# Performance work log

Hardware: AMD Instinct MI355X
Metric: run time of the kernel (lower is better)

The kernel has to match this reference:

```python
import jax, jax.numpy as jnp
import numpy as np

SCALE = 10.0
DIM = 512
DIM_HEAD = 64
HEADS = DIM // DIM_HEAD
LN_EPS = 1e-05
L2_EPS = 1e-12


def l2norm(t, axis=1):
    # Faithful to source: default axis=1 (token axis for [b, n, h, d] tensors)
    denom = jnp.clip(jnp.linalg.norm(t, ord=2, axis=axis, keepdims=True), L2_EPS)
    return t / denom


def setup_inputs() -> dict:
    key = jax.random.key(0)
    k1, k2, k3 = jax.random.split(key, 3)
    B, H, W, C = 8, 32, 32, 512
    x = jax.random.normal(k1, (B, H, W, C), dtype=jnp.float32)
    ln_scale = jnp.ones((C,), dtype=jnp.float32)
    # 1x1 convs == channel matmuls; fan-in scaled init
    w_qkv = jax.random.normal(k2, (C, 3 * DIM), dtype=jnp.float32) / np.sqrt(C)
    w_out = jax.random.normal(k3, (DIM, C), dtype=jnp.float32) / np.sqrt(DIM)
    b_out = jnp.zeros((C,), dtype=jnp.float32)
    return {"x": x, "ln_scale": ln_scale, "w_qkv": w_qkv, "w_out": w_out, "b_out": b_out}


def reference(x, ln_scale, w_qkv, w_out, b_out):
    B, H, W, C = x.shape
    N = H * W
    # LayerNorm over channels (use_bias=False, use_scale=True)
    mean = jnp.mean(x, axis=-1, keepdims=True)
    var = jnp.mean(jnp.square(x - mean), axis=-1, keepdims=True)
    y = (x - mean) * jax.lax.rsqrt(var + LN_EPS) * ln_scale
    # 1x1 conv QKV projection (no bias)
    qkv = jnp.einsum('bhwc,cf->bhwf', y, w_qkv)  # [B,H,W,3*DIM]
    q, k, v = jnp.split(qkv, 3, axis=-1)
    # b x y (h d) -> b (x y) h d
    def to_tokens(t):
        return t.reshape(B, N, HEADS, DIM_HEAD)
    q, k, v = map(to_tokens, (q, k, v))
    # l2norm over axis=1 (token axis), faithful to source default
    q = l2norm(q)
    k = l2norm(k)
    sim = jnp.einsum('bihd,bjhd->bhij', q, k) * SCALE  # [B,heads,N,N]
    attn = jax.nn.softmax(sim, axis=-1)
    out = jnp.einsum('bhij,bjhd->bhid', attn, v)  # [B,heads,N,d]
    # b h (x y) d -> b x y (h d)
    out = out.transpose(0, 2, 1, 3).reshape(B, H, W, HEADS * DIM_HEAD)
    # 1x1 output conv (with bias)
    out = jnp.einsum('bhwf,fc->bhwc', out, w_out) + b_out
    return out
```

## Files before the change

kernel.cpp:

```cpp
#include <hip/hip_runtime.h>

typedef __bf16 bf16x8 __attribute__((ext_vector_type(8)));
typedef float f32x4 __attribute__((ext_vector_type(4)));
typedef float f32x16 __attribute__((ext_vector_type(16)));

#define DEV static __device__ __forceinline__

DEV unsigned short f2bf(float f) {
    union { __bf16 h; unsigned short s; } c; c.h = (__bf16)f; return c.s;
}
DEV float bf2f(unsigned short h) {
    union { unsigned u; float f; } c; c.u = ((unsigned)h) << 16; return c.f;
}
DEV unsigned packbf2(float a, float b) {
    union { __bf16 h[2]; unsigned u; } c;
    c.h[0] = (__bf16)a; c.h[1] = (__bf16)b; return c.u;
}

DEV f32x4 mfma16(bf16x8 a, bf16x8 b, f32x4 c) {
    return __builtin_amdgcn_mfma_f32_16x16x32_bf16(a, b, c, 0, 0, 0);
}
DEV f32x16 mfma32(bf16x8 a, bf16x8 b, f32x16 c) {
    return __builtin_amdgcn_mfma_f32_32x32x16_bf16(a, b, c, 0, 0, 0);
}

#define GLOAD16(gp, lp)                                                        \
    __builtin_amdgcn_global_load_lds(                                          \
        (const __attribute__((address_space(1))) unsigned int*)(gp),           \
        (__attribute__((address_space(3))) unsigned int*)(lp), 16, 0, 0)

__global__ __launch_bounds__(256) void ln_conv_kernel(const float* __restrict__ x,
                                                      const float* __restrict__ lnsc,
                                                      unsigned short* __restrict__ y,
                                                      float* __restrict__ ssq,
                                                      const float* __restrict__ wqkv,
                                                      const float* __restrict__ wout,
                                                      unsigned short* __restrict__ wqkvt,
                                                      unsigned short* __restrict__ woutt) {
    const int t = threadIdx.x;
    if (blockIdx.x >= 2048) {
        __shared__ __bf16 tile[64][65];
        const int wblk = blockIdx.x - 2048;
        const float* src;
        unsigned short* dst;
        int ldsrc, k0, f0;
        if (wblk < 192) {
            src = wqkv; dst = wqkvt; ldsrc = 1536;
            k0 = (wblk / 24) * 64; f0 = (wblk % 24) * 64;
        } else {
            int w2 = wblk - 192;
            src = wout; dst = woutt; ldsrc = 512;
            k0 = (w2 >> 3) * 64; f0 = (w2 & 7) * 64;
        }
#pragma unroll
        for (int j = 0; j < 16; j++) {
            int idx = t + j * 256;
            int a = idx >> 6, b2 = idx & 63;
            tile[b2][a] = (__bf16)src[(size_t)(k0 + a) * ldsrc + f0 + b2];
        }
        __syncthreads();
#pragma unroll
        for (int j = 0; j < 16; j++) {
            int idx = t + j * 256;
            int fb = idx >> 6, kc = idx & 63;
            union { __bf16 h; unsigned short s; } cv;
            cv.h = tile[fb][kc];
            dst[(size_t)(f0 + fb) * 512 + k0 + kc] = cv.s;
        }
        return;
    }
    if (blockIdx.x < 32) ssq[(blockIdx.x << 8) | t] = 0.0f;
    const int token = blockIdx.x * 4 + (t >> 6);
    const int lane = t & 63;
    const float4* xp = (const float4*)(x + (size_t)token * 512 + lane * 8);
    float4 v0 = xp[0], v1 = xp[1];
    float s = v0.x + v0.y + v0.z + v0.w + v1.x + v1.y + v1.z + v1.w;
    float s2 = v0.x * v0.x + v0.y * v0.y + v0.z * v0.z + v0.w * v0.w +
               v1.x * v1.x + v1.y * v1.y + v1.z * v1.z + v1.w * v1.w;
#pragma unroll
    for (int off = 1; off < 64; off <<= 1) {
        s += __shfl_xor(s, off);
        s2 += __shfl_xor(s2, off);
    }
    const float mean = s * (1.0f / 512.0f);
    const float var = s2 * (1.0f / 512.0f) - mean * mean;
    const float rstd = rsqrtf(var + 1e-5f);
    const float4* sp = (const float4*)(lnsc + lane * 8);
    float4 sc0 = sp[0], sc1 = sp[1];
    union { __bf16 h[8]; uint4 v; } pk;
    pk.h[0] = (__bf16)((v0.x - mean) * rstd * sc0.x);
    pk.h[1] = (__bf16)((v0.y - mean) * rstd * sc0.y);
    pk.h[2] = (__bf16)((v0.z - mean) * rstd * sc0.z);
    pk.h[3] = (__bf16)((v0.w - mean) * rstd * sc0.w);
    pk.h[4] = (__bf16)((v1.x - mean) * rstd * sc1.x);
    pk.h[5] = (__bf16)((v1.y - mean) * rstd * sc1.y);
    pk.h[6] = (__bf16)((v1.z - mean) * rstd * sc1.z);
    pk.h[7] = (__bf16)((v1.w - mean) * rstd * sc1.w);
    *(uint4*)(y + (size_t)token * 512 + lane * 8) = pk.v;
}

template <int WM, int WN, int NCOLS, bool OUT_BF16, bool BIAS, bool SSQ, bool VT,
          bool DB>
__global__ __launch_bounds__(256) void gemm_bt(const unsigned short* __restrict__ A,
                                               const unsigned short* __restrict__ Bt,
                                               void* __restrict__ Cout,
                                               const float* __restrict__ bias,
                                               float* __restrict__ ssq,
                                               unsigned short* __restrict__ vt,
                                               int M, int K) {
    constexpr int BM = 2 * WM, BN = 2 * WN;
    constexpr int ASZ = BM * 64 * 2, BSZ = BN * 64 * 2;
    constexpr int NLA = WM / 16, NLB = WN / 16;
    constexpr int NBUF = DB ? 2 : 1;
    constexpr int STG = NBUF * (ASZ + BSZ);
    constexpr int TTB = VT ? 128 * 136 * 2 : 0;
    constexpr int LDSB = STG > TTB ? STG : TTB;
    __shared__ __align__(16) char smem[LDSB];
    const int t = threadIdx.x;
    const int w = t >> 6, lane = t & 63;
    const int g = lane >> 4, l15 = lane & 15;
    const int wr = w >> 1, wc = w & 1;
    const int bR = blockIdx.x, bC = blockIdx.y;
    f32x4 acc[NLA][NLB] = {};
    const size_t ldb = (size_t)K * 2;
    const char* Ag = (const char*)A + (size_t)bR * BM * ldb;
    const char* Bg = (const char*)Bt + (size_t)bC * BN * ldb;

#define GSTAGE(buf, kt_)                                                            \
    {                                                                               \
        char* Ad = smem + (buf) * (ASZ + BSZ);                                      \
        char* Bd = Ad + ASZ;                                                        \
        _Pragma("unroll") for (int i = 0; i < NLA; i++) {                           \
            int o = i * 4096 + t * 16;                                              \
            int row = o >> 7, kb = (o & 127) ^ ((row & 7) << 4);                    \
            GLOAD16(Ag + (size_t)row * ldb + (size_t)(kt_) * 2 + kb, Ad + o);       \
        }                                                                           \
        _Pragma("unroll") for (int i = 0; i < NLB; i++) {                           \
            int o = i * 4096 + t * 16;                                              \
            int row = o >> 7, kb = (o & 127) ^ ((row & 7) << 4);                    \
            GLOAD16(Bg + (size_t)row * ldb + (size_t)(kt_) * 2 + kb, Bd + o);       \
        }                                                                           \
    }

#define GCOMPUTE(buf)                                                               \
    {                                                                               \
        const char* Ab = smem + (buf) * (ASZ + BSZ);                                \
        const char* Bb = Ab + ASZ;                                                  \
        _Pragma("unroll") for (int kk = 0; kk < 64; kk += 32) {                     \
            bf16x8 a[NLA], bb[NLB];                                                 \
            _Pragma("unroll") for (int m = 0; m < NLA; m++) {                       \
                int row = wr * WM + m * 16 + l15;                                   \
                int kb = ((kk + g * 8) * 2) ^ ((row & 7) << 4);                     \
                a[m] = *(const bf16x8*)(Ab + row * 128 + kb);                       \
            }                                                                       \
            _Pragma("unroll") for (int n = 0; n < NLB; n++) {                       \
                int row = wc * WN + n * 16 + l15;                                   \
                int kb = ((kk + g * 8) * 2) ^ ((row & 7) << 4);                     \
                bb[n] = *(const bf16x8*)(Bb + row * 128 + kb);                      \
            }                                                                       \
            _Pragma("unroll") for (int m = 0; m < NLA; m++)                         \
                _Pragma("unroll") for (int n = 0; n < NLB; n++)                     \
                    acc[m][n] = mfma16(a[m], bb[n], acc[m][n]);                     \
        }                                                                           \
    }

    const int NT = K >> 6;
    if constexpr (DB) {
        GSTAGE(0, 0)
        for (int tt = 0; tt < NT; ++tt) {
            const int cur = tt & 1;
            if (tt + 1 < NT) {
                GSTAGE(cur ^ 1, (tt + 1) * 64)
                asm volatile("s_waitcnt vmcnt(%0)" ::"n"(NLA + NLB) : "memory");
            } else {
                asm volatile("s_waitcnt vmcnt(0)" ::: "memory");
            }
            __builtin_amdgcn_s_barrier();
            GCOMPUTE(cur)
            __builtin_amdgcn_s_barrier();
        }
    } else {
        for (int tt = 0; tt < NT; ++tt) {
            __syncthreads();
            GSTAGE(0, tt * 64)
            asm volatile("s_waitcnt vmcnt(0)" ::: "memory");
            __syncthreads();
            GCOMPUTE(0)
        }
    }
#undef GSTAGE
#undef GCOMPUTE

    const int rbase = bR * BM + wr * WM;
    const int cbase = bC * BN + wc * WN;
    if (!VT || bC < 8) {
#pragma unroll
        for (int m = 0; m < NLA; m++)
#pragma unroll
            for (int n = 0; n < NLB; n++)
#pragma unroll
                for (int r = 0; r < 4; r++) {
                    int row = rbase + m * 16 + g * 4 + r;
                    int col = cbase + n * 16 + l15;
                    float v = acc[m][n][r];
                    if constexpr (OUT_BF16)
                        ((unsigned short*)Cout)[(size_t)row * NCOLS + col] = f2bf(v);
                    else
                        ((float*)Cout)[(size_t)row * NCOLS + col] =
                            v + (BIAS ? bias[col] : 0.f);
                }
    }
    if constexpr (SSQ) {
        if (bC < 8) {
            const int bb2 = bR >> 3;
#pragma unroll
            for (int n = 0; n < NLB; n++) {
                float ps = 0.f;
#pragma unroll
                for (int m = 0; m < NLA; m++)
#pragma unroll
                    for (int r = 0; r < 4; r++) ps += acc[m][n][r] * acc[m][n][r];
                ps += __shfl_xor(ps, 16);
                ps += __shfl_xor(ps, 32);
                if (g == 0)
                    atomicAdd(&ssq[bb2 * 1024 + cbase + n * 16 + l15], ps);
            }
        }
    }
    if constexpr (VT) {
        if (bC >= 8) {
            unsigned short* TT = (unsigned short*)smem;
            __syncthreads();
#pragma unroll
            for (int m = 0; m < NLA; m++)
#pragma unroll
                for (int n = 0; n < NLB; n++)
#pragma unroll
                    for (int r = 0; r < 4; r++) {
                        int row = wr * WM + m * 16 + g * 4 + r;
                        int col = wc * WN + n * 16 + l15;
                        TT[col * 136 + row] = f2bf(acc[m][n][r]);
                    }
            __syncthreads();
            const int f = t >> 1, th = t & 1;
            const int fh = (bC - 8) * 128 + f;
            const int hh = fh >> 6, dd = fh & 63;
            const int bb3 = bR >> 3, nb = (bR & 7) * 128;
            unsigned short* dst =
                vt + (((size_t)bb3 * 8 + hh) * 64 + dd) * 1024 + nb + th * 64;
            const unsigned short* srcp = TT + f * 136 + th * 64;
#pragma unroll
            for (int j = 0; j < 8; j++)
                *(uint4*)(dst + j * 8) = *(const uint4*)(srcp + j * 8);
        }
    }
}

__global__ __launch_bounds__(256) void attn_kernel(const unsigned short* __restrict__ qkv,
                                                   const unsigned short* __restrict__ vt,
                                                   unsigned short* __restrict__ attnout,
                                                   const float* __restrict__ ssq) {
    __shared__ unsigned short Ks[2][4096];
    __shared__ unsigned short Vs[2][4096];
    __shared__ float smq[64];
    const int t = threadIdx.x, w = t >> 6, lane = t & 63;
    const int hi = lane >> 5, q31 = lane & 31;
    const int qt = blockIdx.y, bh = blockIdx.x;
    const int b = bh >> 3, h = bh & 7;
    const size_t qrow0 = (size_t)b * 1024 + qt * 128;
    const char* qg = (const char*)qkv;
    const char* vg = (const char*)vt;

    if (t < 64) {
        float nq = fmaxf(sqrtf(ssq[b * 1024 + h * 64 + t]), 1e-12f);
        float nk = fmaxf(sqrtf(ssq[b * 1024 + 512 + h * 64 + t]), 1e-12f);
        smq[t] = 14.42695040888963f / (nq * nk);
    }
    __syncthreads();

    bf16x8 qf[4];
#pragma unroll
    for (int ds = 0; ds < 4; ds++) {
        union { bf16x8 v; unsigned short u[8]; } in, ov;
        in.v = *(const bf16x8*)(qkv + (qrow0 + w * 32 + q31) * 1536 + h * 64 +
                                ds * 16 + hi * 8);
#pragma unroll
        for (int j = 0; j < 8; j++)
            ov.u[j] = f2bf(bf2f(in.u[j]) * smq[ds * 16 + hi * 8 + j]);
        qf[ds] = ov.v;
    }

    f32x16 accO[2] = {};
    float prs = 0.f;

#define ASTAGE(buf, tt_)                                                              \
    {                                                                                 \
        const int kt_ = (tt_) * 64;                                                   \
        _Pragma("unroll") for (int i = 0; i < 2; i++) {                               \
            int o = i * 4096 + t * 16;                                                \
            int row = o >> 7, kb = (o & 127) ^ ((row & 7) << 4);                      \
            GLOAD16(qg + ((size_t)b * 1024 + kt_ + row) * 3072 + 1024 + h * 128 + kb, \
                    (char*)Ks[buf] + o);                                              \
            GLOAD16(vg + ((size_t)bh * 64 + row) * 2048 + (size_t)kt_ * 2 + kb,       \
                    (char*)Vs[buf] + o);                                              \
        }                                                                             \
    }

    ASTAGE(0, 0)
    for (int tt = 0; tt < 16; ++tt) {
        const int cur = tt & 1;
        if (tt < 15) {
            ASTAGE(cur ^ 1, tt + 1)
            asm volatile("s_waitcnt vmcnt(4)" ::: "memory");
        } else {
            asm volatile("s_waitcnt vmcnt(0)" ::: "memory");
        }
        __builtin_amdgcn_s_barrier();

#pragma unroll
        for (int kvb = 0; kvb < 2; kvb++) {
            f32x16 sa = {};
            __builtin_amdgcn_s_setprio(1);
#pragma unroll
            for (int ds = 0; ds < 4; ds++) {
                const int krow = kvb * 32 + q31;
                const int kb = ((ds * 16 + hi * 8) * 2) ^ ((krow & 7) << 4);
                bf16x8 kf = *(const bf16x8*)((const char*)Ks[cur] + krow * 128 + kb);
                sa = mfma32(kf, qf[ds], sa);
            }
            __builtin_amdgcn_s_setprio(0);
            float p[16];
#pragma unroll
            for (int r = 0; r < 16; r++) {
                p[r] = __builtin_amdgcn_exp2f(sa[r]);
                prs += p[r];
            }
            bf16x8 pf[2];
#pragma unroll
            for (int s2 = 0; s2 < 2; s2++) {
                unsigned a0 = packbf2(p[s2 * 8 + 0], p[s2 * 8 + 1]);
                unsigned a1 = packbf2(p[s2 * 8 + 2], p[s2 * 8 + 3]);
                unsigned b0 = packbf2(p[s2 * 8 + 4], p[s2 * 8 + 5]);
                unsigned b1 = packbf2(p[s2 * 8 + 6], p[s2 * 8 + 7]);
                asm volatile("v_permlane32_swap_b32 %0, %1" : "+v"(a0), "+v"(b0));
                asm volatile("v_permlane32_swap_b32 %0, %1" : "+v"(a1), "+v"(b1));
                union { unsigned u[4]; bf16x8 v; } fr;
                fr.u[0] = a0; fr.u[1] = a1; fr.u[2] = b0; fr.u[3] = b1;
                pf[s2] = fr.v;
            }
            __builtin_amdgcn_s_setprio(1);
#pragma unroll
            for (int s2 = 0; s2 < 2; s2++)
#pragma unroll
                for (int dvb = 0; dvb < 2; dvb++) {
                    const int vrow = dvb * 32 + q31;
                    const int kb =
                        ((kvb * 32 + s2 * 16 + hi * 8) * 2) ^ ((vrow & 7) << 4);
                    bf16x8 vf = *(const bf16x8*)((const char*)Vs[cur] + vrow * 128 + kb);
                    accO[dvb] = mfma32(vf, pf[s2], accO[dvb]);
                }
            __builtin_amdgcn_s_setprio(0);
        }
        __builtin_amdgcn_s_barrier();
    }
#undef ASTAGE

    const float tot = prs + __shfl_xor(prs, 32);
    const float inv = 1.0f / tot;
    unsigned short* orow = attnout + (qrow0 + w * 32 + q31) * 512 + h * 64;
#pragma unroll
    for (int dvb = 0; dvb < 2; dvb++)
#pragma unroll
        for (int grp = 0; grp < 4; grp++) {
            float f0 = accO[dvb][grp * 4 + 0] * inv;
            float f1 = accO[dvb][grp * 4 + 1] * inv;
            float f2 = accO[dvb][grp * 4 + 2] * inv;
            float f3 = accO[dvb][grp * 4 + 3] * inv;
            uint2 pk;
            pk.x = packbf2(f0, f1);
            pk.y = packbf2(f2, f3);
            *(uint2*)(orow + dvb * 32 + grp * 8 + 4 * hi) = pk;
        }
}

extern "C" void kernel_launch(void* const* d_in, const int* in_sizes, int n_in,
                              void* d_out, int out_size, void* d_ws, size_t ws_size,
                              hipStream_t stream) {
    const float* x = (const float*)d_in[0];
    const float* ln_scale = (const float*)d_in[1];
    const float* w_qkv = (const float*)d_in[2];
    const float* w_out = (const float*)d_in[3];
    const float* b_out = (const float*)d_in[4];
    float* out = (float*)d_out;

    char* ws = (char*)d_ws;
    unsigned short* y = (unsigned short*)(ws + 0);
    unsigned short* wqkvt = (unsigned short*)(ws + 8388608);
    unsigned short* woutt = (unsigned short*)(ws + 9961472);
    unsigned short* qkv = (unsigned short*)(ws + 10485760);
    unsigned short* vt = (unsigned short*)(ws + 35651584);
    float* ssq = (float*)(ws + 44040192);
    unsigned short* attnout = (unsigned short*)(ws + 0);

    ln_conv_kernel<<<2304, 256, 0, stream>>>(x, ln_scale, y, ssq, w_qkv, w_out, wqkvt,
                                             woutt);
    gemm_bt<64, 64, 1536, true, false, true, true, false>
        <<<dim3(64, 12), 256, 0, stream>>>(y, wqkvt, qkv, nullptr, ssq, vt, 8192, 512);
    attn_kernel<<<dim3(64, 8), 256, 0, stream>>>(qkv, vt, attnout, ssq);
    gemm_bt<32, 64, 512, false, true, false, false, true>
        <<<dim3(128, 4), 256, 0, stream>>>(attnout, woutt, out, b_out, nullptr, nullptr,
                                           8192, 512);
}
```

Baseline: 71.81 us.

## Process two 32-row query blocks per wave in attention to reuse K/V fragments

Each attention block now covers 256 query rows instead of 128, with every wave handling two 32-row query sub-blocks. The K and V fragments are loaded from LDS once per kv-block and reused for both sub-blocks, which halves LDS reads and global K/V staging per query row. In exchange the grid drops from 512 to 256 blocks, which lowers occupancy and parallelism on a large GPU, and register pressure rises from the doubled accumulators and query fragments.

```diff
diff --git a/kernel.cpp b/kernel.cpp
--- a/kernel.cpp
+++ b/kernel.cpp
@@ -267,7 +267,7 @@
     const int hi = lane >> 5, q31 = lane & 31;
     const int qt = blockIdx.y, bh = blockIdx.x;
     const int b = bh >> 3, h = bh & 7;
-    const size_t qrow0 = (size_t)b * 1024 + qt * 128;
+    const size_t qrow0 = (size_t)b * 1024 + qt * 256;
     const char* qg = (const char*)qkv;
     const char* vg = (const char*)vt;
 
@@ -278,20 +278,22 @@
     }
     __syncthreads();
 
-    bf16x8 qf[4];
-#pragma unroll
-    for (int ds = 0; ds < 4; ds++) {
-        union { bf16x8 v; unsigned short u[8]; } in, ov;
-        in.v = *(const bf16x8*)(qkv + (qrow0 + w * 32 + q31) * 1536 + h * 64 +
-                                ds * 16 + hi * 8);
-#pragma unroll
-        for (int j = 0; j < 8; j++)
-            ov.u[j] = f2bf(bf2f(in.u[j]) * smq[ds * 16 + hi * 8 + j]);
-        qf[ds] = ov.v;
-    }
-
-    f32x16 accO[2] = {};
-    float prs = 0.f;
+    bf16x8 qf[2][4];
+#pragma unroll
+    for (int qb = 0; qb < 2; qb++)
+#pragma unroll
+        for (int ds = 0; ds < 4; ds++) {
+            union { bf16x8 v; unsigned short u[8]; } in, ov;
+            in.v = *(const bf16x8*)(qkv + (qrow0 + w * 64 + qb * 32 + q31) * 1536 +
+                                    h * 64 + ds * 16 + hi * 8);
+#pragma unroll
+            for (int j = 0; j < 8; j++)
+                ov.u[j] = f2bf(bf2f(in.u[j]) * smq[ds * 16 + hi * 8 + j]);
+            qf[qb][ds] = ov.v;
+        }
+
+    f32x16 accO[2][2] = {};
+    float prs[2] = {0.f, 0.f};
 
 #define ASTAGE(buf, tt_)                                                              \
     {                                                                                 \
@@ -319,36 +321,14 @@
 
 #pragma unroll
         for (int kvb = 0; kvb < 2; kvb++) {
-            f32x16 sa = {};
-            __builtin_amdgcn_s_setprio(1);
+            bf16x8 kf[4];
 #pragma unroll
             for (int ds = 0; ds < 4; ds++) {
                 const int krow = kvb * 32 + q31;
                 const int kb = ((ds * 16 + hi * 8) * 2) ^ ((krow & 7) << 4);
-                bf16x8 kf = *(const bf16x8*)((const char*)Ks[cur] + krow * 128 + kb);
-                sa = mfma32(kf, qf[ds], sa);
+                kf[ds] = *(const bf16x8*)((const char*)Ks[cur] + krow * 128 + kb);
             }
-            __builtin_amdgcn_s_setprio(0);
-            float p[16];
-#pragma unroll
-            for (int r = 0; r < 16; r++) {
-                p[r] = __builtin_amdgcn_exp2f(sa[r]);
-                prs += p[r];
-            }
-            bf16x8 pf[2];
-#pragma unroll
-            for (int s2 = 0; s2 < 2; s2++) {
-                unsigned a0 = packbf2(p[s2 * 8 + 0], p[s2 * 8 + 1]);
-                unsigned a1 = packbf2(p[s2 * 8 + 2], p[s2 * 8 + 3]);
-                unsigned b0 = packbf2(p[s2 * 8 + 4], p[s2 * 8 + 5]);
-                unsigned b1 = packbf2(p[s2 * 8 + 6], p[s2 * 8 + 7]);
-                asm volatile("v_permlane32_swap_b32 %0, %1" : "+v"(a0), "+v"(b0));
-                asm volatile("v_permlane32_swap_b32 %0, %1" : "+v"(a1), "+v"(b1));
-                union { unsigned u[4]; bf16x8 v; } fr;
-                fr.u[0] = a0; fr.u[1] = a1; fr.u[2] = b0; fr.u[3] = b1;
-                pf[s2] = fr.v;
-            }
-            __builtin_amdgcn_s_setprio(1);
+            bf16x8 vfr[2][2];
 #pragma unroll
             for (int s2 = 0; s2 < 2; s2++)
 #pragma unroll
@@ -356,31 +336,68 @@
                     const int vrow = dvb * 32 + q31;
                     const int kb =
                         ((kvb * 32 + s2 * 16 + hi * 8) * 2) ^ ((vrow & 7) << 4);
-                    bf16x8 vf = *(const bf16x8*)((const char*)Vs[cur] + vrow * 128 + kb);
-                    accO[dvb] = mfma32(vf, pf[s2], accO[dvb]);
+                    vfr[s2][dvb] =
+                        *(const bf16x8*)((const char*)Vs[cur] + vrow * 128 + kb);
                 }
-            __builtin_amdgcn_s_setprio(0);
+#pragma unroll
+            for (int qb = 0; qb < 2; qb++) {
+                f32x16 sa = {};
+                __builtin_amdgcn_s_setprio(1);
+#pragma unroll
+                for (int ds = 0; ds < 4; ds++) sa = mfma32(kf[ds], qf[qb][ds], sa);
+                __builtin_amdgcn_s_setprio(0);
+                float p[16];
+#pragma unroll
+                for (int r = 0; r < 16; r++) {
+                    p[r] = __builtin_amdgcn_exp2f(sa[r]);
+                    prs[qb] += p[r];
+                }
+                bf16x8 pf[2];
+#pragma unroll
+                for (int s2 = 0; s2 < 2; s2++) {
+                    unsigned a0 = packbf2(p[s2 * 8 + 0], p[s2 * 8 + 1]);
+                    unsigned a1 = packbf2(p[s2 * 8 + 2], p[s2 * 8 + 3]);
+                    unsigned b0 = packbf2(p[s2 * 8 + 4], p[s2 * 8 + 5]);
+                    unsigned b1 = packbf2(p[s2 * 8 + 6], p[s2 * 8 + 7]);
+                    asm volatile("v_permlane32_swap_b32 %0, %1" : "+v"(a0), "+v"(b0));
+                    asm volatile("v_permlane32_swap_b32 %0, %1" : "+v"(a1), "+v"(b1));
+                    union { unsigned u[4]; bf16x8 v; } fr;
+                    fr.u[0] = a0; fr.u[1] = a1; fr.u[2] = b0; fr.u[3] = b1;
+                    pf[s2] = fr.v;
+                }
+                __builtin_amdgcn_s_setprio(1);
+#pragma unroll
+                for (int s2 = 0; s2 < 2; s2++)
+#pragma unroll
+                    for (int dvb = 0; dvb < 2; dvb++)
+                        accO[qb][dvb] = mfma32(vfr[s2][dvb], pf[s2], accO[qb][dvb]);
+                __builtin_amdgcn_s_setprio(0);
+            }
         }
         __builtin_amdgcn_s_barrier();
     }
 #undef ASTAGE
 
-    const float tot = prs + __shfl_xor(prs, 32);
-    const float inv = 1.0f / tot;
-    unsigned short* orow = attnout + (qrow0 + w * 32 + q31) * 512 + h * 64;
-#pragma unroll
-    for (int dvb = 0; dvb < 2; dvb++)
-#pragma unroll
-        for (int grp = 0; grp < 4; grp++) {
-            float f0 = accO[dvb][grp * 4 + 0] * inv;
-            float f1 = accO[dvb][grp * 4 + 1] * inv;
-            float f2 = accO[dvb][grp * 4 + 2] * inv;
-            float f3 = accO[dvb][grp * 4 + 3] * inv;
-            uint2 pk;
-            pk.x = packbf2(f0, f1);
-            pk.y = packbf2(f2, f3);
-            *(uint2*)(orow + dvb * 32 + grp * 8 + 4 * hi) = pk;
-        }
+#pragma unroll
+    for (int qb = 0; qb < 2; qb++) {
+        const float tot = prs[qb] + __shfl_xor(prs[qb], 32);
+        const float inv = 1.0f / tot;
+        unsigned short* orow =
+            attnout + (qrow0 + w * 64 + qb * 32 + q31) * 512 + h * 64;
+#pragma unroll
+        for (int dvb = 0; dvb < 2; dvb++)
+#pragma unroll
+            for (int grp = 0; grp < 4; grp++) {
+                float f0 = accO[qb][dvb][grp * 4 + 0] * inv;
+                float f1 = accO[qb][dvb][grp * 4 + 1] * inv;
+                float f2 = accO[qb][dvb][grp * 4 + 2] * inv;
+                float f3 = accO[qb][dvb][grp * 4 + 3] * inv;
+                uint2 pk;
+                pk.x = packbf2(f0, f1);
+                pk.y = packbf2(f2, f3);
+                *(uint2*)(orow + dvb * 32 + grp * 8 + 4 * hi) = pk;
+            }
+    }
 }
 
 extern "C" void kernel_launch(void* const* d_in, const int* in_sizes, int n_in,
@@ -406,7 +423,7 @@
                                              woutt);
     gemm_bt<64, 64, 1536, true, false, true, true, false>
         <<<dim3(64, 12), 256, 0, stream>>>(y, wqkvt, qkv, nullptr, ssq, vt, 8192, 512);
-    attn_kernel<<<dim3(64, 8), 256, 0, stream>>>(qkv, vt, attnout, ssq);
+    attn_kernel<<<dim3(64, 4), 256, 0, stream>>>(qkv, vt, attnout, ssq);
     gemm_bt<32, 64, 512, false, true, false, false, true>
         <<<dim3(128, 4), 256, 0, stream>>>(attnout, woutt, out, b_out, nullptr, nullptr,
                                            8192, 512);
```

New measurement: 76.01 us. +5.8%, slower.

## Store K and V in MFMA-fragment-major layouts so attention loads are contiguous

Applied to the files above, without the earlier changes.

The QKV GEMM epilogue now writes Q to its own buffer and transposes K and V through LDS into per-head, fragment-major layouts, 16-byte chunks ordered by k-slice then token. The attention kernel can then stage K/V tiles with fully contiguous per-wave global loads and read LDS fragments without XOR swizzling. This aims to cut strided global traffic and address math in the attention loop. In exchange the GEMM epilogue does more LDS transpose work for K blocks, and the unswizzled LDS reads may hit bank conflicts.

```diff
diff --git a/kernel.cpp b/kernel.cpp
--- a/kernel.cpp
+++ b/kernel.cpp
@@ -99,21 +99,21 @@
     *(uint4*)(y + (size_t)token * 512 + lane * 8) = pk.v;
 }
 
-template <int WM, int WN, int NCOLS, bool OUT_BF16, bool BIAS, bool SSQ, bool VT,
-          bool DB>
+template <int WM, int WN, int NCOLS, bool OUT_BF16, bool BIAS, bool QKV, bool DB>
 __global__ __launch_bounds__(256) void gemm_bt(const unsigned short* __restrict__ A,
                                                const unsigned short* __restrict__ Bt,
                                                void* __restrict__ Cout,
                                                const float* __restrict__ bias,
                                                float* __restrict__ ssq,
-                                               unsigned short* __restrict__ vt,
+                                               unsigned short* __restrict__ kst,
+                                               unsigned short* __restrict__ vst,
                                                int M, int K) {
     constexpr int BM = 2 * WM, BN = 2 * WN;
     constexpr int ASZ = BM * 64 * 2, BSZ = BN * 64 * 2;
     constexpr int NLA = WM / 16, NLB = WN / 16;
     constexpr int NBUF = DB ? 2 : 1;
     constexpr int STG = NBUF * (ASZ + BSZ);
-    constexpr int TTB = VT ? 128 * 136 * 2 : 0;
+    constexpr int TTB = QKV ? 128 * 136 * 2 : 0;
     constexpr int LDSB = STG > TTB ? STG : TTB;
     __shared__ __align__(16) char smem[LDSB];
     const int t = threadIdx.x;
@@ -193,7 +193,7 @@
 
     const int rbase = bR * BM + wr * WM;
     const int cbase = bC * BN + wc * WN;
-    if (!VT || bC < 8) {
+    if (!QKV || bC < 4) {
 #pragma unroll
         for (int m = 0; m < NLA; m++)
 #pragma unroll
@@ -210,7 +210,7 @@
                             v + (BIAS ? bias[col] : 0.f);
                 }
     }
-    if constexpr (SSQ) {
+    if constexpr (QKV) {
         if (bC < 8) {
             const int bb2 = bR >> 3;
 #pragma unroll
@@ -226,10 +226,9 @@
                     atomicAdd(&ssq[bb2 * 1024 + cbase + n * 16 + l15], ps);
             }
         }
-    }
-    if constexpr (VT) {
-        if (bC >= 8) {
+        if (bC >= 4) {
             unsigned short* TT = (unsigned short*)smem;
+            const bool isK = bC < 8;
             __syncthreads();
 #pragma unroll
             for (int m = 0; m < NLA; m++)
@@ -239,25 +238,41 @@
                     for (int r = 0; r < 4; r++) {
                         int row = wr * WM + m * 16 + g * 4 + r;
                         int col = wc * WN + n * 16 + l15;
-                        TT[col * 136 + row] = f2bf(acc[m][n][r]);
+                        if (isK)
+                            TT[row * 136 + col] = f2bf(acc[m][n][r]);
+                        else
+                            TT[col * 136 + row] = f2bf(acc[m][n][r]);
                     }
             __syncthreads();
-            const int f = t >> 1, th = t & 1;
-            const int fh = (bC - 8) * 128 + f;
-            const int hh = fh >> 6, dd = fh & 63;
-            const int bb3 = bR >> 3, nb = (bR & 7) * 128;
-            unsigned short* dst =
-                vt + (((size_t)bb3 * 8 + hh) * 64 + dd) * 1024 + nb + th * 64;
-            const unsigned short* srcp = TT + f * 136 + th * 64;
-#pragma unroll
-            for (int j = 0; j < 8; j++)
-                *(uint4*)(dst + j * 8) = *(const uint4*)(srcp + j * 8);
-        }
-    }
-}
-
-__global__ __launch_bounds__(256) void attn_kernel(const unsigned short* __restrict__ qkv,
-                                                   const unsigned short* __restrict__ vt,
+            const int b2 = bR >> 3, rb = bR & 7;
+            if (isK) {
+#pragma unroll
+                for (int j = 0; j < 8; j++) {
+                    int sl = (t >> 7) + j * 2;
+                    int nl = t & 127;
+                    int hh = (bC - 4) * 2 + (sl >> 3), s = sl & 7;
+                    *(uint4*)(kst +
+                              (((size_t)(b2 * 8 + hh) * 8 + s) * 1024 + rb * 128 + nl) *
+                                  8) = *(const uint4*)(TT + nl * 136 + sl * 8);
+                }
+            } else {
+#pragma unroll
+                for (int j = 0; j < 8; j++) {
+                    int fl = t & 127;
+                    int svl = (t >> 7) + j * 2;
+                    int hh = (bC - 8) * 2 + (fl >> 6), d = fl & 63;
+                    *(uint4*)(vst +
+                              (((size_t)(b2 * 8 + hh) * 128 + rb * 16 + svl) * 64 + d) *
+                                  8) = *(const uint4*)(TT + fl * 136 + svl * 8);
+                }
+            }
+        }
+    }
+}
+
+__global__ __launch_bounds__(256) void attn_kernel(const unsigned short* __restrict__ qbuf,
+                                                   const unsigned short* __restrict__ kst,
+                                                   const unsigned short* __restrict__ vst,
                                                    unsigned short* __restrict__ attnout,
                                                    const float* __restrict__ ssq) {
     __shared__ unsigned short Ks[2][4096];
@@ -268,8 +283,8 @@
     const int qt = blockIdx.y, bh = blockIdx.x;
     const int b = bh >> 3, h = bh & 7;
     const size_t qrow0 = (size_t)b * 1024 + qt * 128;
-    const char* qg = (const char*)qkv;
-    const char* vg = (const char*)vt;
+    const char* kstb = (const char*)kst + (size_t)bh * 131072;
+    const char* vstb = (const char*)vst + (size_t)bh * 131072;
 
     if (t < 64) {
         float nq = fmaxf(sqrtf(ssq[b * 1024 + h * 64 + t]), 1e-12f);
@@ -282,7 +297,7 @@
 #pragma unroll
     for (int ds = 0; ds < 4; ds++) {
         union { bf16x8 v; unsigned short u[8]; } in, ov;
-        in.v = *(const bf16x8*)(qkv + (qrow0 + w * 32 + q31) * 1536 + h * 64 +
+        in.v = *(const bf16x8*)(qbuf + (qrow0 + w * 32 + q31) * 512 + h * 64 +
                                 ds * 16 + hi * 8);
 #pragma unroll
         for (int j = 0; j < 8; j++)
@@ -293,17 +308,16 @@
     f32x16 accO[2] = {};
     float prs = 0.f;
 
-#define ASTAGE(buf, tt_)                                                              \
-    {                                                                                 \
-        const int kt_ = (tt_) * 64;                                                   \
-        _Pragma("unroll") for (int i = 0; i < 2; i++) {                               \
-            int o = i * 4096 + t * 16;                                                \
-            int row = o >> 7, kb = (o & 127) ^ ((row & 7) << 4);                      \
-            GLOAD16(qg + ((size_t)b * 1024 + kt_ + row) * 3072 + 1024 + h * 128 + kb, \
-                    (char*)Ks[buf] + o);                                              \
-            GLOAD16(vg + ((size_t)bh * 64 + row) * 2048 + (size_t)kt_ * 2 + kb,       \
-                    (char*)Vs[buf] + o);                                              \
-        }                                                                             \
+#define ASTAGE(buf, tt_)                                                            \
+    {                                                                               \
+        _Pragma("unroll") for (int i = 0; i < 2; i++) {                             \
+            const int s = i * 4 + w;                                                \
+            const int o = i * 4096 + t * 16;                                        \
+            GLOAD16(kstb + (((size_t)s * 1024 + (tt_) * 64 + lane) << 4),           \
+                    (char*)Ks[buf] + o);                                            \
+            GLOAD16(vstb + (((size_t)(tt_) * 512 + s * 64 + lane) << 4),            \
+                    (char*)Vs[buf] + o);                                            \
+        }                                                                           \
     }
 
     ASTAGE(0, 0)
@@ -323,9 +337,9 @@
             __builtin_amdgcn_s_setprio(1);
 #pragma unroll
             for (int ds = 0; ds < 4; ds++) {
-                const int krow = kvb * 32 + q31;
-                const int kb = ((ds * 16 + hi * 8) * 2) ^ ((krow & 7) << 4);
-                bf16x8 kf = *(const bf16x8*)((const char*)Ks[cur] + krow * 128 + kb);
+                bf16x8 kf = *(const bf16x8*)((const char*)Ks[cur] +
+                                             ((ds * 2 + hi) << 10) +
+                                             ((kvb * 32 + q31) << 4));
                 sa = mfma32(kf, qf[ds], sa);
             }
             __builtin_amdgcn_s_setprio(0);
@@ -353,10 +367,9 @@
             for (int s2 = 0; s2 < 2; s2++)
 #pragma unroll
                 for (int dvb = 0; dvb < 2; dvb++) {
-                    const int vrow = dvb * 32 + q31;
-                    const int kb =
-                        ((kvb * 32 + s2 * 16 + hi * 8) * 2) ^ ((vrow & 7) << 4);
-                    bf16x8 vf = *(const bf16x8*)((const char*)Vs[cur] + vrow * 128 + kb);
+                    bf16x8 vf = *(const bf16x8*)((const char*)Vs[cur] +
+                                                 ((kvb * 4 + s2 * 2 + hi) << 10) +
+                                                 ((dvb * 32 + q31) << 4));
                     accO[dvb] = mfma32(vf, pf[s2], accO[dvb]);
                 }
             __builtin_amdgcn_s_setprio(0);
@@ -397,17 +410,19 @@
     unsigned short* y = (unsigned short*)(ws + 0);
     unsigned short* wqkvt = (unsigned short*)(ws + 8388608);
     unsigned short* woutt = (unsigned short*)(ws + 9961472);
-    unsigned short* qkv = (unsigned short*)(ws + 10485760);
-    unsigned short* vt = (unsigned short*)(ws + 35651584);
-    float* ssq = (float*)(ws + 44040192);
+    unsigned short* qbuf = (unsigned short*)(ws + 10485760);
+    unsigned short* kst = (unsigned short*)(ws + 18874368);
+    unsigned short* vst = (unsigned short*)(ws + 27262976);
+    float* ssq = (float*)(ws + 35651584);
     unsigned short* attnout = (unsigned short*)(ws + 0);
 
     ln_conv_kernel<<<2304, 256, 0, stream>>>(x, ln_scale, y, ssq, w_qkv, w_out, wqkvt,
                                              woutt);
-    gemm_bt<64, 64, 1536, true, false, true, true, false>
-        <<<dim3(64, 12), 256, 0, stream>>>(y, wqkvt, qkv, nullptr, ssq, vt, 8192, 512);
-    attn_kernel<<<dim3(64, 8), 256, 0, stream>>>(qkv, vt, attnout, ssq);
-    gemm_bt<32, 64, 512, false, true, false, false, true>
+    gemm_bt<64, 64, 512, true, false, true, false>
+        <<<dim3(64, 12), 256, 0, stream>>>(y, wqkvt, qbuf, nullptr, ssq, kst, vst,
+                                           8192, 512);
+    attn_kernel<<<dim3(64, 8), 256, 0, stream>>>(qbuf, kst, vst, attnout, ssq);
+    gemm_bt<32, 64, 512, false, true, false, true>
         <<<dim3(128, 4), 256, 0, stream>>>(attnout, woutt, out, b_out, nullptr, nullptr,
-                                           8192, 512);
-}
+                                           nullptr, 8192, 512);
+}
```

Measured after the change: 71.40 us. Within noise of the previous version (-0.6%).
